# Kernel optimization log

Hardware: AMD Instinct MI355X
Metric: run time of the kernel (lower is better)

## Reference

```python
import jax, jax.numpy as jnp
import numpy as np

B, N, E, H = 2, 2048, 1024, 16
D = E // H  # head_dim = 64


def setup_inputs() -> dict:
    key = jax.random.key(0)
    ks = jax.random.split(key, 8)
    s = 1.0 / np.sqrt(D)
    return {
        "query": jax.random.normal(ks[0], (B, N, E), jnp.float32),
        "key": jax.random.normal(ks[1], (B, N, E), jnp.float32),
        "value": jax.random.normal(ks[2], (B, N, E), jnp.float32),
        "mask": jax.random.randint(ks[3], (B, N), 0, 2, jnp.int32),
        # per-head Linear weights, torch layout (out_features, in_features) stacked over heads
        "Wq": jax.random.uniform(ks[4], (H, D, D), jnp.float32, -s, s),
        "Wk": jax.random.uniform(ks[5], (H, D, D), jnp.float32, -s, s),
        "Wv": jax.random.uniform(ks[6], (H, D, D), jnp.float32, -s, s),
        "Wo": jax.random.uniform(ks[7], (E, E), jnp.float32, -1.0 / np.sqrt(E), 1.0 / np.sqrt(E)),
    }


def reference(query, key, value, mask, Wq, Wk, Wv, Wo):
    b, n, e = query.shape
    h, d, _ = Wq.shape
    q = query.reshape(b, n, h, d)
    k = key.reshape(b, n, h, d)
    v = value.reshape(b, n, h, d)
    # per-head Linear (no bias): x @ W[i].T, batched over heads
    qh = jnp.einsum('bnhd,hed->bnhe', q, Wq)
    kh = jnp.einsum('bnhd,hed->bnhe', k, Wk)
    vh = jnp.einsum('bnhd,hed->bnhe', v, Wv)
    # NOTE: original scales by sqrt(embed_size), not sqrt(head_dim)
    scores = jnp.einsum('bqhd,bkhd->bhqk', qh, kh) / (e ** 0.5)
    # NOTE: mask is unsqueezed on the KEY axis position in torch (dim=2),
    # so it masks entire QUERY rows, broadcasting over keys.
    scores = jnp.where(mask[:, None, :, None] == 0, jnp.float32(-1e28), scores)
    probs = jax.nn.softmax(scores, axis=-1)
    attn = jnp.einsum('bhqk,bkhd->bqhd', probs, vh).reshape(b, n, e)
    return attn @ Wo.T
```

## Files before the change

kernel.cpp:

```cpp
#include <hip/hip_runtime.h>
#include <hip/hip_bf16.h>

#define B_ 2
#define N_ 2048
#define E_ 1024
#define H_ 16
#define D_ 64
#define BH_ (B_ * H_)

typedef __attribute__((ext_vector_type(4))) float f32x4;
typedef __attribute__((ext_vector_type(8))) short bf16x8;
typedef __attribute__((ext_vector_type(4))) short s16x4;
typedef __attribute__((ext_vector_type(4))) int i32x4;

#define MFMA(a, b, c) __builtin_amdgcn_mfma_f32_16x16x32_bf16(a, b, c, 0, 0, 0)

#define AS1(p) ((const __attribute__((address_space(1))) unsigned int*)(p))
#define AS3(p) ((__attribute__((address_space(3))) unsigned int*)(p))

static __device__ __forceinline__ unsigned short f2bf(float f) {
    unsigned int u = __builtin_bit_cast(unsigned int, f);
    u += 0x7fff + ((u >> 16) & 1);
    return (unsigned short)(u >> 16);
}
static __device__ __forceinline__ float bf2f(unsigned short s) {
    unsigned int u = ((unsigned int)s) << 16;
    return __builtin_bit_cast(float, u);
}
static __device__ __forceinline__ int pack2bf(float lo, float hi) {
    return (int)f2bf(lo) | ((int)f2bf(hi) << 16);
}
static __device__ __forceinline__ bf16x8 cvt8s(const float* __restrict__ p, float sc) {
    f32x4 a = *(const f32x4*)p;
    f32x4 b = *(const f32x4*)(p + 4);
    bf16x8 r;
    r[0] = (short)f2bf(a.x * sc); r[1] = (short)f2bf(a.y * sc);
    r[2] = (short)f2bf(a.z * sc); r[3] = (short)f2bf(a.w * sc);
    r[4] = (short)f2bf(b.x * sc); r[5] = (short)f2bf(b.y * sc);
    r[6] = (short)f2bf(b.z * sc); r[7] = (short)f2bf(b.w * sc);
    return r;
}

__global__ __launch_bounds__(256, 4)
void proj_kernel(const float* __restrict__ q, const float* __restrict__ k,
                 const float* __restrict__ v,
                 const float* __restrict__ Wq, const float* __restrict__ Wk,
                 const float* __restrict__ Wv,
                 const int* __restrict__ mask,
                 unsigned short* __restrict__ qh, unsigned short* __restrict__ kh,
                 unsigned short* __restrict__ vt) {
    const int z = blockIdx.z;
    const float* X = (z == 0) ? q : (z == 1) ? k : v;
    const float* W = (z == 0) ? Wq : (z == 1) ? Wk : Wv;
    unsigned short* out = (z == 0) ? qh : (z == 1) ? kh : vt;
    const float wscale = (z == 0) ? (1.44269504f * 0.03125f) : 1.0f;

    const int lane = threadIdx.x & 63;
    const int wave = threadIdx.x >> 6;
    const int l16  = lane & 15;
    const int quad = lane >> 4;
    const int bh = blockIdx.y;
    const int b = bh >> 4, h = bh & 15;
    const int n0 = blockIdx.x * 64;
    const int tok = n0 + wave * 16 + l16;

    const float* xrow = X + ((size_t)(b * N_ + tok)) * E_ + h * 64;
    bf16x8 xf[2];
    xf[0] = cvt8s(xrow + quad * 8, 1.0f);
    xf[1] = cvt8s(xrow + 32 + quad * 8, 1.0f);

    const float* Wh = W + (size_t)h * 64 * 64;
    bf16x8 wf[4][2];
#pragma unroll
    for (int t4 = 0; t4 < 4; ++t4) {
        const float* wrow = Wh + (t4 * 16 + l16) * 64;
        wf[t4][0] = cvt8s(wrow + quad * 8, wscale);
        wf[t4][1] = cvt8s(wrow + 32 + quad * 8, wscale);
    }

    const int mk = (z == 0) ? mask[b * N_ + tok] : 1;

#pragma unroll
    for (int mi = 0; mi < 4; ++mi) {
        f32x4 a = {0.f, 0.f, 0.f, 0.f};
        a = MFMA(wf[mi][0], xf[0], a);
        a = MFMA(wf[mi][1], xf[1], a);
        if (z != 2) {
            s16x4 pk = {(short)f2bf(a.x), (short)f2bf(a.y),
                        (short)f2bf(a.z), (short)f2bf(a.w)};
            if (!mk) pk = (s16x4){0, 0, 0, 0};
            *(s16x4*)(out + ((size_t)bh * N_ + tok) * 64 + mi * 16 + quad * 4) = pk;
        } else {
#pragma unroll
            for (int r = 0; r < 4; ++r) {
                int dout = mi * 16 + quad * 4 + r;
                out[((size_t)bh * 64 + dout) * N_ + tok] = (unsigned short)f2bf(a[r]);
            }
        }
    }
}

__global__ __launch_bounds__(256)
void cvt_wo_kernel(const float* __restrict__ wo, unsigned short* __restrict__ wob) {
    int idx = blockIdx.x * 256 + threadIdx.x;
    f32x4 v = *(const f32x4*)(wo + (size_t)idx * 4);
    s16x4 r = {(short)f2bf(v.x), (short)f2bf(v.y), (short)f2bf(v.z), (short)f2bf(v.w)};
    *(s16x4*)(wob + (size_t)idx * 4) = r;
}

__global__ __launch_bounds__(256, 2)
void attn_kernel(const unsigned short* __restrict__ qh,
                 const unsigned short* __restrict__ kh,
                 const unsigned short* __restrict__ vt,
                 unsigned short* __restrict__ attnb) {
    __shared__ short Kb[2][64][72];
    __shared__ short Vb[2][64][72];

    const int tid  = threadIdx.x;
    const int lane = tid & 63;
    const int wave = tid >> 6;
    const int l16  = lane & 15;
    const int quad = lane >> 4;

    const int flat = blockIdx.y * gridDim.x + blockIdx.x;
    const int qblk = flat >> 5;
    const int rem  = flat & 31;
    const int bh   = ((rem & 7) << 2) | (rem >> 3);
    const int b = bh >> 4, h = bh & 15;
    const int q0 = qblk * 128 + wave * 32;

    const unsigned short* kbase = kh + (size_t)bh * N_ * 64;
    const unsigned short* vbase = vt + (size_t)bh * 64 * N_;

    const int c0i = tid;
    const int c1i = tid + 256;

    const int srcA = (((quad * 2) & 3) << 4) + l16;
    const int srcB = (((quad * 2 + 1) & 3) << 4) + l16;
    const bool hiSel = (quad >= 2);

    bf16x8 qf[2][2];
#pragma unroll
    for (int qi = 0; qi < 2; ++qi) {
        const unsigned short* qrow = qh + ((size_t)bh * N_ + q0 + qi * 16 + l16) * 64;
        qf[qi][0] = *(const bf16x8*)(qrow + quad * 8);
        qf[qi][1] = *(const bf16x8*)(qrow + 32 + quad * 8);
    }

    float lI[2] = {0.f, 0.f};
    f32x4 o[4][2];
#pragma unroll
    for (int mi = 0; mi < 4; ++mi)
#pragma unroll
        for (int qi = 0; qi < 2; ++qi) o[mi][qi] = (f32x4){0.f, 0.f, 0.f, 0.f};

    bf16x8 gK0, gK1, gV0, gV1;
    gK0 = *(const bf16x8*)(kbase + c0i * 8);
    gK1 = *(const bf16x8*)(kbase + c1i * 8);
    gV0 = *(const bf16x8*)(vbase + (size_t)(c0i >> 3) * N_ + (c0i & 7) * 8);
    gV1 = *(const bf16x8*)(vbase + (size_t)(c1i >> 3) * N_ + (c1i & 7) * 8);
    *(bf16x8*)(&Kb[0][c0i >> 3][(c0i & 7) * 8]) = gK0;
    *(bf16x8*)(&Kb[0][c1i >> 3][(c1i & 7) * 8]) = gK1;
    *(bf16x8*)(&Vb[0][c0i >> 3][(c0i & 7) * 8]) = gV0;
    *(bf16x8*)(&Vb[0][c1i >> 3][(c1i & 7) * 8]) = gV1;
    __syncthreads();

    for (int kt = 0; kt < N_ / 64; ++kt) {
        const int cur = kt & 1;

        if (kt + 1 < N_ / 64) {
            const int k0n = (kt + 1) * 64;
            gK0 = *(const bf16x8*)(kbase + (size_t)k0n * 64 + c0i * 8);
            gK1 = *(const bf16x8*)(kbase + (size_t)k0n * 64 + c1i * 8);
            gV0 = *(const bf16x8*)(vbase + (size_t)(c0i >> 3) * N_ + k0n + (c0i & 7) * 8);
            gV1 = *(const bf16x8*)(vbase + (size_t)(c1i >> 3) * N_ + k0n + (c1i & 7) * 8);
        }

        bf16x8 ka[4][2];
#pragma unroll
        for (int t4 = 0; t4 < 4; ++t4) {
            ka[t4][0] = *(const bf16x8*)(&Kb[cur][t4 * 16 + l16][quad * 8]);
            ka[t4][1] = *(const bf16x8*)(&Kb[cur][t4 * 16 + l16][32 + quad * 8]);
        }

        f32x4 s[2][4];
#pragma unroll
        for (int qi = 0; qi < 2; ++qi)
#pragma unroll
            for (int t4 = 0; t4 < 4; ++t4) {
                f32x4 z = {0.f, 0.f, 0.f, 0.f};
                z = MFMA(ka[t4][0], qf[qi][0], z);
                z = MFMA(ka[t4][1], qf[qi][1], z);
                s[qi][t4] = z;
            }

        bf16x8 va[4][2];
#pragma unroll
        for (int mi = 0; mi < 4; ++mi) {
            va[mi][0] = *(const bf16x8*)(&Vb[cur][mi * 16 + l16][quad * 8]);
            va[mi][1] = *(const bf16x8*)(&Vb[cur][mi * 16 + l16][32 + quad * 8]);
        }

#pragma unroll
        for (int qi = 0; qi < 2; ++qi) {
            float rsum = 0.f;
            int pk[4][2];
#pragma unroll
            for (int t4 = 0; t4 < 4; ++t4) {
                f32x4 p;
#pragma unroll
                for (int r = 0; r < 4; ++r) {
                    p[r] = __builtin_amdgcn_exp2f(s[qi][t4][r]);
                    rsum += p[r];
                }
                pk[t4][0] = pack2bf(p.x, p.y);
                pk[t4][1] = pack2bf(p.z, p.w);
            }
            rsum += __shfl_xor(rsum, 16);
            rsum += __shfl_xor(rsum, 32);
            lI[qi] += rsum;

            i32x4 w0, w1;
#pragma unroll
            for (int d = 0; d < 2; ++d) {
                int a0 = __shfl(pk[0][d], srcA), a1 = __shfl(pk[1][d], srcA);
                int b0 = __shfl(pk[0][d], srcB), b1 = __shfl(pk[1][d], srcB);
                w0[d]     = hiSel ? a1 : a0;
                w0[2 + d] = hiSel ? b1 : b0;
                int c0 = __shfl(pk[2][d], srcA), c1 = __shfl(pk[3][d], srcA);
                int e0 = __shfl(pk[2][d], srcB), e1 = __shfl(pk[3][d], srcB);
                w1[d]     = hiSel ? c1 : c0;
                w1[2 + d] = hiSel ? e1 : e0;
            }
            bf16x8 pb0 = __builtin_bit_cast(bf16x8, w0);
            bf16x8 pb1 = __builtin_bit_cast(bf16x8, w1);

#pragma unroll
            for (int mi = 0; mi < 4; ++mi) {
                o[mi][qi] = MFMA(va[mi][0], pb0, o[mi][qi]);
                o[mi][qi] = MFMA(va[mi][1], pb1, o[mi][qi]);
            }
        }

        if (kt + 1 < N_ / 64) {
            const int nxt = cur ^ 1;
            *(bf16x8*)(&Kb[nxt][c0i >> 3][(c0i & 7) * 8]) = gK0;
            *(bf16x8*)(&Kb[nxt][c1i >> 3][(c1i & 7) * 8]) = gK1;
            *(bf16x8*)(&Vb[nxt][c0i >> 3][(c0i & 7) * 8]) = gV0;
            *(bf16x8*)(&Vb[nxt][c1i >> 3][(c1i & 7) * 8]) = gV1;
            __syncthreads();
        }
    }

#pragma unroll
    for (int qi = 0; qi < 2; ++qi) {
        const float inv = 1.0f / lI[qi];
        const int qrow_idx = q0 + qi * 16 + l16;
#pragma unroll
        for (int mi = 0; mi < 4; ++mi) {
            f32x4 ov = o[mi][qi];
            s16x4 pkk = {(short)f2bf(ov.x * inv), (short)f2bf(ov.y * inv),
                         (short)f2bf(ov.z * inv), (short)f2bf(ov.w * inv)};
            int d0 = mi * 16 + quad * 4;
            *(s16x4*)(attnb + ((size_t)(b * N_ + qrow_idx)) * E_ + h * 64 + d0) = pkk;
        }
    }
}

__global__ __launch_bounds__(256, 2)
void out_gemm_kernel(const unsigned short* __restrict__ A,
                     const unsigned short* __restrict__ Bw,
                     float* __restrict__ out) {
    __shared__ short As[2][128 * 32];
    __shared__ short Bs[2][128 * 32];

    const int tid  = threadIdx.x;
    const int lane = tid & 63;
    const int wave = tid >> 6;
    const int l16  = lane & 15;
    const int quad = lane >> 4;
    const int wm = wave & 1, wn = wave >> 1;
    const int m0 = blockIdx.x * 128;
    const int n0 = blockIdx.y * 128;

    const unsigned short* gA = A + (size_t)m0 * E_;
    const unsigned short* gB = Bw + (size_t)n0 * E_;

    f32x4 acc[4][4];
#pragma unroll
    for (int mt = 0; mt < 4; ++mt)
#pragma unroll
        for (int nt = 0; nt < 4; ++nt) acc[mt][nt] = (f32x4){0.f, 0.f, 0.f, 0.f};

#define OG_STAGE(buf, k0)                                                        \
    {                                                                            \
        _Pragma("unroll")                                                        \
        for (int j = 0; j < 2; ++j) {                                            \
            const int p = j * 256 + wave * 64 + lane;                            \
            const int c = p >> 7, r = p & 127;                                   \
            const int lb = (j * 256 + wave * 64) * 8;                            \
            __builtin_amdgcn_global_load_lds(                                    \
                AS1(gA + (size_t)r * E_ + (k0) + c * 8),                         \
                AS3(&As[buf][lb]), 16, 0, 0);                                    \
            __builtin_amdgcn_global_load_lds(                                    \
                AS1(gB + (size_t)r * E_ + (k0) + c * 8),                         \
                AS3(&Bs[buf][lb]), 16, 0, 0);                                    \
        }                                                                        \
    }

    OG_STAGE(0, 0)
    __syncthreads();

    for (int kt = 0; kt < E_ / 32; ++kt) {
        const int cur = kt & 1;
        if (kt + 1 < E_ / 32) OG_STAGE(cur ^ 1, (kt + 1) * 32)

        bf16x8 af[4], bf[4];
#pragma unroll
        for (int mt = 0; mt < 4; ++mt)
            af[mt] = *(const bf16x8*)(&As[cur][(quad * 128 + wm * 64 + mt * 16 + l16) * 8]);
#pragma unroll
        for (int nt = 0; nt < 4; ++nt)
            bf[nt] = *(const bf16x8*)(&Bs[cur][(quad * 128 + wn * 64 + nt * 16 + l16) * 8]);

#pragma unroll
        for (int mt = 0; mt < 4; ++mt)
#pragma unroll
            for (int nt = 0; nt < 4; ++nt)
                acc[mt][nt] = MFMA(af[mt], bf[nt], acc[mt][nt]);

        __syncthreads();
    }

#pragma unroll
    for (int mt = 0; mt < 4; ++mt)
#pragma unroll
        for (int nt = 0; nt < 4; ++nt)
#pragma unroll
            for (int r = 0; r < 4; ++r)
                out[(size_t)(m0 + wm * 64 + mt * 16 + quad * 4 + r) * E_ +
                    n0 + wn * 64 + nt * 16 + l16] = acc[mt][nt][r];
#undef OG_STAGE
}

extern "C" void kernel_launch(void* const* d_in, const int* in_sizes, int n_in,
                              void* d_out, int out_size, void* d_ws, size_t ws_size,
                              hipStream_t stream) {
    const float* q    = (const float*)d_in[0];
    const float* k    = (const float*)d_in[1];
    const float* v    = (const float*)d_in[2];
    const int*   mask = (const int*)d_in[3];
    const float* Wq   = (const float*)d_in[4];
    const float* Wk   = (const float*)d_in[5];
    const float* Wv   = (const float*)d_in[6];
    const float* Wo   = (const float*)d_in[7];
    float* out = (float*)d_out;

    char* ws = (char*)d_ws;
    unsigned short* qh    = (unsigned short*)(ws);
    unsigned short* kh    = (unsigned short*)(ws + (size_t)8 * 1024 * 1024);
    unsigned short* vt    = (unsigned short*)(ws + (size_t)16 * 1024 * 1024);
    unsigned short* attnb = (unsigned short*)(ws + (size_t)24 * 1024 * 1024);
    unsigned short* wob   = (unsigned short*)(ws);

    dim3 blk(256);
    proj_kernel<<<dim3(N_ / 64, BH_, 3), blk, 0, stream>>>(q, k, v, Wq, Wk, Wv, mask,
                                                           qh, kh, vt);
    attn_kernel<<<dim3(16, 32), blk, 0, stream>>>(qh, kh, vt, attnb);
    cvt_wo_kernel<<<dim3(E_ * E_ / 1024), blk, 0, stream>>>(Wo, wob);
    out_gemm_kernel<<<dim3(32, 8), blk, 0, stream>>>(attnb, wob, out);
}
```

Measured before the change: 224.2 us.

## Reorganize attention LDS tiles chunk-major and use 8 waves in output GEMM

The attention kernel's K/V shared-memory tiles move from a padded row-major layout to a chunk-major layout, where each 8-element column chunk is stored contiguously across all 64 rows. The MFMA fragment reads become contiguous per quad, which is meant to cut LDS bank conflicts and drop the padding. Separately, the output GEMM goes from 256 to 512 threads per block with 8 waves, each computing a 64x32 sub-tile. That halves the accumulators per wave and gives each thread one global_load_lds per operand, trading per-wave register use for more waves per tile.

```diff
diff --git a/kernel.cpp b/kernel.cpp
--- a/kernel.cpp
+++ b/kernel.cpp
@@ -113,8 +113,8 @@
                  const unsigned short* __restrict__ kh,
                  const unsigned short* __restrict__ vt,
                  unsigned short* __restrict__ attnb) {
-    __shared__ short Kb[2][64][72];
-    __shared__ short Vb[2][64][72];
+    __shared__ short Kb[2][4096];
+    __shared__ short Vb[2][4096];
 
     const int tid  = threadIdx.x;
     const int lane = tid & 63;
@@ -134,6 +134,8 @@
 
     const int c0i = tid;
     const int c1i = tid + 256;
+    const int l0 = ((c0i & 7) * 64 + (c0i >> 3)) * 8;
+    const int l1 = ((c1i & 7) * 64 + (c1i >> 3)) * 8;
 
     const int srcA = (((quad * 2) & 3) << 4) + l16;
     const int srcB = (((quad * 2 + 1) & 3) << 4) + l16;
@@ -159,10 +161,10 @@
     gK1 = *(const bf16x8*)(kbase + c1i * 8);
     gV0 = *(const bf16x8*)(vbase + (size_t)(c0i >> 3) * N_ + (c0i & 7) * 8);
     gV1 = *(const bf16x8*)(vbase + (size_t)(c1i >> 3) * N_ + (c1i & 7) * 8);
-    *(bf16x8*)(&Kb[0][c0i >> 3][(c0i & 7) * 8]) = gK0;
-    *(bf16x8*)(&Kb[0][c1i >> 3][(c1i & 7) * 8]) = gK1;
-    *(bf16x8*)(&Vb[0][c0i >> 3][(c0i & 7) * 8]) = gV0;
-    *(bf16x8*)(&Vb[0][c1i >> 3][(c1i & 7) * 8]) = gV1;
+    *(bf16x8*)(&Kb[0][l0]) = gK0;
+    *(bf16x8*)(&Kb[0][l1]) = gK1;
+    *(bf16x8*)(&Vb[0][l0]) = gV0;
+    *(bf16x8*)(&Vb[0][l1]) = gV1;
     __syncthreads();
 
     for (int kt = 0; kt < N_ / 64; ++kt) {
@@ -179,8 +181,8 @@
         bf16x8 ka[4][2];
 #pragma unroll
         for (int t4 = 0; t4 < 4; ++t4) {
-            ka[t4][0] = *(const bf16x8*)(&Kb[cur][t4 * 16 + l16][quad * 8]);
-            ka[t4][1] = *(const bf16x8*)(&Kb[cur][t4 * 16 + l16][32 + quad * 8]);
+            ka[t4][0] = *(const bf16x8*)(&Kb[cur][(quad * 64 + t4 * 16 + l16) * 8]);
+            ka[t4][1] = *(const bf16x8*)(&Kb[cur][((4 + quad) * 64 + t4 * 16 + l16) * 8]);
         }
 
         f32x4 s[2][4];
@@ -197,8 +199,8 @@
         bf16x8 va[4][2];
 #pragma unroll
         for (int mi = 0; mi < 4; ++mi) {
-            va[mi][0] = *(const bf16x8*)(&Vb[cur][mi * 16 + l16][quad * 8]);
-            va[mi][1] = *(const bf16x8*)(&Vb[cur][mi * 16 + l16][32 + quad * 8]);
+            va[mi][0] = *(const bf16x8*)(&Vb[cur][(quad * 64 + mi * 16 + l16) * 8]);
+            va[mi][1] = *(const bf16x8*)(&Vb[cur][((4 + quad) * 64 + mi * 16 + l16) * 8]);
         }
 
 #pragma unroll
@@ -244,10 +246,10 @@
 
         if (kt + 1 < N_ / 64) {
             const int nxt = cur ^ 1;
-            *(bf16x8*)(&Kb[nxt][c0i >> 3][(c0i & 7) * 8]) = gK0;
-            *(bf16x8*)(&Kb[nxt][c1i >> 3][(c1i & 7) * 8]) = gK1;
-            *(bf16x8*)(&Vb[nxt][c0i >> 3][(c0i & 7) * 8]) = gV0;
-            *(bf16x8*)(&Vb[nxt][c1i >> 3][(c1i & 7) * 8]) = gV1;
+            *(bf16x8*)(&Kb[nxt][l0]) = gK0;
+            *(bf16x8*)(&Kb[nxt][l1]) = gK1;
+            *(bf16x8*)(&Vb[nxt][l0]) = gV0;
+            *(bf16x8*)(&Vb[nxt][l1]) = gV1;
             __syncthreads();
         }
     }
@@ -267,7 +269,7 @@
     }
 }
 
-__global__ __launch_bounds__(256, 2)
+__global__ __launch_bounds__(512, 1)
 void out_gemm_kernel(const unsigned short* __restrict__ A,
                      const unsigned short* __restrict__ Bw,
                      float* __restrict__ out) {
@@ -276,9 +278,9 @@
 
     const int tid  = threadIdx.x;
     const int lane = tid & 63;
-    const int wave = tid >> 6;
     const int l16  = lane & 15;
     const int quad = lane >> 4;
+    const int wave = tid >> 6;
     const int wm = wave & 1, wn = wave >> 1;
     const int m0 = blockIdx.x * 128;
     const int n0 = blockIdx.y * 128;
@@ -286,26 +288,19 @@
     const unsigned short* gA = A + (size_t)m0 * E_;
     const unsigned short* gB = Bw + (size_t)n0 * E_;
 
-    f32x4 acc[4][4];
+    f32x4 acc[4][2];
 #pragma unroll
     for (int mt = 0; mt < 4; ++mt)
 #pragma unroll
-        for (int nt = 0; nt < 4; ++nt) acc[mt][nt] = (f32x4){0.f, 0.f, 0.f, 0.f};
-
+        for (int nt = 0; nt < 2; ++nt) acc[mt][nt] = (f32x4){0.f, 0.f, 0.f, 0.f};
+
+    const int cc = tid >> 7, rr = tid & 127;
 #define OG_STAGE(buf, k0)                                                        \
     {                                                                            \
-        _Pragma("unroll")                                                        \
-        for (int j = 0; j < 2; ++j) {                                            \
-            const int p = j * 256 + wave * 64 + lane;                            \
-            const int c = p >> 7, r = p & 127;                                   \
-            const int lb = (j * 256 + wave * 64) * 8;                            \
-            __builtin_amdgcn_global_load_lds(                                    \
-                AS1(gA + (size_t)r * E_ + (k0) + c * 8),                         \
-                AS3(&As[buf][lb]), 16, 0, 0);                                    \
-            __builtin_amdgcn_global_load_lds(                                    \
-                AS1(gB + (size_t)r * E_ + (k0) + c * 8),                         \
-                AS3(&Bs[buf][lb]), 16, 0, 0);                                    \
-        }                                                                        \
+        __builtin_amdgcn_global_load_lds(AS1(gA + (size_t)rr * E_ + (k0) + cc * 8), \
+                                         AS3(&As[buf][tid * 8]), 16, 0, 0);      \
+        __builtin_amdgcn_global_load_lds(AS1(gB + (size_t)rr * E_ + (k0) + cc * 8), \
+                                         AS3(&Bs[buf][tid * 8]), 16, 0, 0);      \
     }
 
     OG_STAGE(0, 0)
@@ -315,18 +310,18 @@
         const int cur = kt & 1;
         if (kt + 1 < E_ / 32) OG_STAGE(cur ^ 1, (kt + 1) * 32)
 
-        bf16x8 af[4], bf[4];
+        bf16x8 af[4], bf[2];
 #pragma unroll
         for (int mt = 0; mt < 4; ++mt)
             af[mt] = *(const bf16x8*)(&As[cur][(quad * 128 + wm * 64 + mt * 16 + l16) * 8]);
 #pragma unroll
-        for (int nt = 0; nt < 4; ++nt)
-            bf[nt] = *(const bf16x8*)(&Bs[cur][(quad * 128 + wn * 64 + nt * 16 + l16) * 8]);
+        for (int nt = 0; nt < 2; ++nt)
+            bf[nt] = *(const bf16x8*)(&Bs[cur][(quad * 128 + wn * 32 + nt * 16 + l16) * 8]);
 
 #pragma unroll
         for (int mt = 0; mt < 4; ++mt)
 #pragma unroll
-            for (int nt = 0; nt < 4; ++nt)
+            for (int nt = 0; nt < 2; ++nt)
                 acc[mt][nt] = MFMA(af[mt], bf[nt], acc[mt][nt]);
 
         __syncthreads();
@@ -335,11 +330,11 @@
 #pragma unroll
     for (int mt = 0; mt < 4; ++mt)
 #pragma unroll
-        for (int nt = 0; nt < 4; ++nt)
+        for (int nt = 0; nt < 2; ++nt)
 #pragma unroll
             for (int r = 0; r < 4; ++r)
                 out[(size_t)(m0 + wm * 64 + mt * 16 + quad * 4 + r) * E_ +
-                    n0 + wn * 64 + nt * 16 + l16] = acc[mt][nt][r];
+                    n0 + wn * 32 + nt * 16 + l16] = acc[mt][nt][r];
 #undef OG_STAGE
 }
 
@@ -368,5 +363,5 @@
                                                            qh, kh, vt);
     attn_kernel<<<dim3(16, 32), blk, 0, stream>>>(qh, kh, vt, attnb);
     cvt_wo_kernel<<<dim3(E_ * E_ / 1024), blk, 0, stream>>>(Wo, wob);
-    out_gemm_kernel<<<dim3(32, 8), blk, 0, stream>>>(attnb, wob, out);
-}
+    out_gemm_kernel<<<dim3(32, 8), dim3(512), 0, stream>>>(attnb, wob, out);
+}
```

New measurement: 237.1 us. +5.8%, slower.
